# Performance work log

Hardware: AMD Instinct MI355X
Metric: run time of the kernel (lower is better)

Reference implementation:

```python
import jax, jax.numpy as jnp
import numpy as np

N, E, F, H, G = 50000, 800000, 128, 32, 64  # nodes, edges, feat, hidden, graphs


def _p(k, shape):
    return (jax.random.normal(k, shape, jnp.float32) / np.sqrt(shape[0])).astype(jnp.float32)


def setup_inputs() -> dict:
    key = jax.random.key(0)
    ks = jax.random.split(key, 24)
    x = jax.random.normal(ks[0], (N, F), jnp.float32)
    edge_index = jax.random.randint(ks[1], (2, E), 0, N, dtype=jnp.int32)
    batch = jnp.sort(jax.random.randint(ks[2], (N,), 0, G, dtype=jnp.int32))
    d = {"x": x, "edge_index": edge_index, "batch": batch}
    # GATv2 conv params: (Wl, Wr, att vector a, bias) per layer; dims 128->32->64->128
    dims = [(F, H), (H, 2 * H), (2 * H, 4 * H)]
    i = 3
    for li, (din, dout) in enumerate(dims, 1):
        d[f"Wl{li}"] = _p(ks[i], (din, dout)); i += 1
        d[f"Wr{li}"] = _p(ks[i], (din, dout)); i += 1
        d[f"a{li}"] = _p(ks[i], (dout,)); i += 1
        d[f"b{li}"] = jnp.zeros((dout,), jnp.float32)
    # MLP head 128->1024->512->128->32->4
    mdims = [(4 * H, 1024), (1024, 512), (512, 128), (128, 32), (32, 4)]
    for li, (din, dout) in enumerate(mdims, 1):
        d[f"mw{li}"] = _p(ks[i], (din, dout)); i += 1
        d[f"mb{li}"] = jnp.zeros((dout,), jnp.float32)
    return d


def _gatv2(x, Wl, Wr, a, b, src, dst, n):
    # GATv2: e = a . LeakyReLU(Wl x_src + Wr x_dst), softmax over incoming edges of dst
    xl = x @ Wl
    xr = x @ Wr
    e = jax.nn.leaky_relu(xl[src] + xr[dst], 0.2) @ a  # [E]
    m = jax.ops.segment_max(e, dst, num_segments=n)
    ex = jnp.exp(e - m[dst])
    denom = jax.ops.segment_sum(ex, dst, num_segments=n)
    alpha = ex / (denom[dst] + 1e-16)
    return jax.ops.segment_sum(alpha[:, None] * xl[src], dst, num_segments=n) + b


def reference(x, edge_index, batch,
              Wl1, Wr1, a1, b1, Wl2, Wr2, a2, b2, Wl3, Wr3, a3, b3,
              mw1, mb1, mw2, mb2, mw3, mb3, mw4, mb4, mw5, mb5):
    src, dst = edge_index[0], edge_index[1]
    n = x.shape[0]
    h = _gatv2(x, Wl1, Wr1, a1, b1, src, dst, n)
    h = jax.nn.leaky_relu(h, 0.01)
    h = _gatv2(h, Wl2, Wr2, a2, b2, src, dst, n)
    h = jax.nn.leaky_relu(h, 0.01)
    h = _gatv2(h, Wl3, Wr3, a3, b3, src, dst, n)
    # global max pool per graph
    g = jax.ops.segment_max(h, batch, num_segments=G)  # [G, 4H]
    g = jax.nn.relu(g @ mw1 + mb1)
    g = jax.nn.relu(g @ mw2 + mb2)
    g = jax.nn.relu(g @ mw3 + mb3)
    g = jax.nn.relu(g @ mw4 + mb4)
    return g @ mw5 + mb5  # [G, 4]
```

## Files before the change

kernel.cpp:

```cpp
#include <hip/hip_runtime.h>
#include <cfloat>

#define N_NODES 50000
#define N_EDGES 800000
#define N_GRAPHS 64
#define POOL_CHUNK 64
#define DEG_BUCKETS 64
#define SCAN_NB ((N_NODES + 255) / 256)

#define BUK_SHIFT 8
#define NBUK ((N_NODES + 255) / 256)
#define CHUNK 4096
#define CAP 6144

typedef _Float16 half8 __attribute__((ext_vector_type(8)));
typedef _Float16 half4 __attribute__((ext_vector_type(4)));


__global__ __launch_bounds__(256) void bucket_hist_kernel(const int* __restrict__ dst,
                                                          int* __restrict__ bhist, int n) {
    __shared__ int lh[NBUK];
    int t = threadIdx.x;
    if (t < NBUK) lh[t] = 0;
    __syncthreads();
    int i0 = blockIdx.x * 1024;
#pragma unroll
    for (int j = 0; j < 4; ++j) {
        int i = i0 + j * 256 + t;
        if (i < n) atomicAdd(&lh[dst[i] >> BUK_SHIFT], 1);
    }
    __syncthreads();
    if (t < NBUK && lh[t]) atomicAdd(&bhist[t], lh[t]);
}

__global__ __launch_bounds__(256) void bucket_scan_kernel(const int* __restrict__ bhist,
                                                          int* __restrict__ bbase,
                                                          int* __restrict__ bcur) {
    __shared__ int sm[256];
    int t = threadIdx.x;
    int v = (t < NBUK) ? bhist[t] : 0;
    sm[t] = v;
    __syncthreads();
    for (int off = 1; off < 256; off <<= 1) {
        int x = (t >= off) ? sm[t - off] : 0;
        __syncthreads();
        sm[t] += x;
        __syncthreads();
    }
    int excl = sm[t] - v;
    if (t < NBUK) { bbase[t] = excl; bcur[t] = excl; }
    if (t == 255) bbase[NBUK] = sm[255];
}


__global__ __launch_bounds__(256) void binscat_kernel(const int* __restrict__ src,
        const int* __restrict__ dst, int* __restrict__ bcur,
        int2* __restrict__ ebuf, int n) {
    __shared__ int2 staged[CHUNK];
    __shared__ int lh[NBUK], lbase[NBUK], lpos[NBUK], gpos[NBUK];
    __shared__ int ssc[256];
    int t = threadIdx.x;
    int e0 = blockIdx.x * CHUNK;
    int len = n - e0; if (len > CHUNK) len = CHUNK; if (len < 0) len = 0;
    if (t < NBUK) { lh[t] = 0; lpos[t] = 0; }
    __syncthreads();
    int s[16], d[16];
#pragma unroll
    for (int j = 0; j < 16; ++j) {
        int i = j * 256 + t;
        if (i < len) {
            s[j] = src[e0 + i];
            d[j] = dst[e0 + i];
            atomicAdd(&lh[d[j] >> BUK_SHIFT], 1);
        } else d[j] = -1;
    }
    __syncthreads();
    int v = (t < NBUK) ? lh[t] : 0;
    ssc[t] = v;
    __syncthreads();
    for (int off = 1; off < 256; off <<= 1) {
        int x = (t >= off) ? ssc[t - off] : 0;
        __syncthreads();
        ssc[t] += x;
        __syncthreads();
    }
    if (t < NBUK) {
        lbase[t] = ssc[t] - v;
        gpos[t] = v ? atomicAdd(&bcur[t], v) : 0;
    }
    __syncthreads();
#pragma unroll
    for (int j = 0; j < 16; ++j) {
        if (d[j] >= 0) {
            int b = d[j] >> BUK_SHIFT;
            int slot = lbase[b] + atomicAdd(&lpos[b], 1);
            staged[slot] = make_int2(s[j], d[j]);
        }
    }
    __syncthreads();
    for (int i = t; i < len; i += 256) {
        int2 p = staged[i];
        int b = p.y >> BUK_SHIFT;
        ebuf[gpos[b] + (i - lbase[b])] = p;
    }
}


__global__ __launch_bounds__(256) void csr_final_kernel(const int2* __restrict__ ebuf,
        const int* __restrict__ bbase, int* __restrict__ rowptr, int* __restrict__ csrc,
        int* __restrict__ deg, int* __restrict__ dhist, int n_nodes, int n_edges) {
    __shared__ int lcnt[256], lbs[256], lpos[256], ssc[256];
    __shared__ int lh64[DEG_BUCKETS];
    __shared__ int buf[CAP];
    int b = blockIdx.x, t = threadIdx.x;
    int nstart = b << BUK_SHIFT;
    int nodes = n_nodes - nstart; if (nodes > 256) nodes = 256;
    int r0 = bbase[b], r1 = bbase[b + 1];
    int len = r1 - r0;
    lcnt[t] = 0;
    lpos[t] = 0;
    if (t < DEG_BUCKETS) lh64[t] = 0;
    __syncthreads();
    for (int i = t; i < len; i += 256)
        atomicAdd(&lcnt[ebuf[r0 + i].y - nstart], 1);
    __syncthreads();
    int v = lcnt[t];
    ssc[t] = v;
    __syncthreads();
    for (int off = 1; off < 256; off <<= 1) {
        int x = (t >= off) ? ssc[t - off] : 0;
        __syncthreads();
        ssc[t] += x;
        __syncthreads();
    }
    lbs[t] = ssc[t] - v;
    if (t < nodes) {
        rowptr[nstart + t] = r0 + lbs[t];
        deg[nstart + t] = v;
        int dd = (v > DEG_BUCKETS - 1) ? DEG_BUCKETS - 1 : v;
        atomicAdd(&lh64[dd], 1);
    }
    if (b == NBUK - 1 && t == 0) rowptr[n_nodes] = n_edges;
    __syncthreads();
    if (t < DEG_BUCKETS && lh64[t]) atomicAdd(&dhist[t], lh64[t]);
    if (len <= CAP) {
        for (int i = t; i < len; i += 256) {
            int2 p = ebuf[r0 + i];
            int dn = p.y - nstart;
            int pos = lbs[dn] + atomicAdd(&lpos[dn], 1);
            buf[pos] = p.x;
        }
        __syncthreads();
        for (int i = t; i < len; i += 256) csrc[r0 + i] = buf[i];
    } else {
        for (int i = t; i < len; i += 256) {
            int2 p = ebuf[r0 + i];
            int dn = p.y - nstart;
            int pos = lbs[dn] + atomicAdd(&lpos[dn], 1);
            csrc[r0 + pos] = p.x;
        }
    }
}


__global__ void dscan_kernel(const int* __restrict__ dhist, int* __restrict__ dcur) {
    int t = threadIdx.x;
    int dv = dhist[t];
    int incl = dv;
    for (int off = 1; off < 64; off <<= 1) {
        int x = __shfl_up(incl, off, 64);
        if (t >= off) incl += x;
    }
    dcur[t] = incl - dv;
}

__global__ __launch_bounds__(256) void perm_kernel(const int* __restrict__ deg,
        int* __restrict__ dcur, int* __restrict__ perm, int n) {
    __shared__ int lh[DEG_BUCKETS], lbase[DEG_BUCKETS];
    int t = threadIdx.x;
    int i = blockIdx.x * 256 + t;
    if (t < DEG_BUCKETS) lh[t] = 0;
    __syncthreads();
    int d = 0, loc = 0;
    bool valid = (i < n);
    if (valid) {
        int v = deg[i];
        d = (v > DEG_BUCKETS - 1) ? DEG_BUCKETS - 1 : v;
        loc = atomicAdd(&lh[d], 1);
    }
    __syncthreads();
    if (t < DEG_BUCKETS) lbase[t] = lh[t] ? atomicAdd(&dcur[t], lh[t]) : 0;
    __syncthreads();
    if (valid) perm[lbase[d] + loc] = i;
}


template<int DIN, int DOUT, int TR, int RPT>
__global__ __launch_bounds__(256) void gemm2_kernel(const float* __restrict__ h,
        const float* __restrict__ Wl, const float* __restrict__ Wr,
        _Float16* __restrict__ xl, _Float16* __restrict__ xr, int n) {
    constexpr int CG = (2 * DOUT) / 4;
    constexpr int RG = 256 / CG;
    static_assert(RG * RPT == TR, "tile rows mismatch");
    static_assert(RPT % 4 == 0, "RPT multiple of 4");
    constexpr int TRP = TR + 4;
    __shared__ float sW[2 * DIN * DOUT];
    __shared__ float sX[DIN * TRP];
    int tid = threadIdx.x;
    for (int i = tid; i < DIN * DOUT; i += 256) {
        sW[i] = Wl[i];
        sW[DIN * DOUT + i] = Wr[i];
    }
    int r0 = blockIdx.x * TR;
    for (int i = tid; i < TR * DIN; i += 256) {
        int row = i / DIN, k = i % DIN;
        float v = (r0 + row < n) ? h[(r0 + row) * DIN + k] : 0.f;
        sX[k * TRP + row] = v;
    }
    __syncthreads();

    int cg = tid % CG, rg = tid / CG;
    int c = cg * 4;
    int sel = (c >= DOUT) ? 1 : 0;
    int cc = c - sel * DOUT;
    const float* wp = sW + sel * DIN * DOUT + cc;
    const float* xp = sX + rg * RPT;

    float acc[RPT][4] = {};
#pragma unroll 4
    for (int k = 0; k < DIN; ++k) {
        float4 wv = *(const float4*)(wp + k * DOUT);
        float wa[4] = {wv.x, wv.y, wv.z, wv.w};
        float xa[RPT];
#pragma unroll
        for (int rr = 0; rr < RPT; rr += 4) {
            float4 xv = *(const float4*)(xp + k * TRP + rr);
            xa[rr + 0] = xv.x; xa[rr + 1] = xv.y; xa[rr + 2] = xv.z; xa[rr + 3] = xv.w;
        }
#pragma unroll
        for (int r = 0; r < RPT; ++r)
#pragma unroll
            for (int q = 0; q < 4; ++q)
                acc[r][q] += xa[r] * wa[q];
    }

    _Float16* obase = sel ? xr : xl;
#pragma unroll
    for (int r = 0; r < RPT; ++r) {
        int row = r0 + rg * RPT + r;
        if (row < n) {
            half4 o = {(_Float16)acc[r][0], (_Float16)acc[r][1],
                       (_Float16)acc[r][2], (_Float16)acc[r][3]};
            *(half4*)(obase + (size_t)row * DOUT + cc) = o;
        }
    }
}

template<int DIN, int DOUT, int TR, int RPT>
__global__ __launch_bounds__(256) void gemm1w_kernel(const float* __restrict__ h,
        const float* __restrict__ Wl, const float* __restrict__ Wr,
        _Float16* __restrict__ xl, _Float16* __restrict__ xr, int n) {
    constexpr int CG = DOUT / 4;
    constexpr int RG = 256 / CG;
    static_assert(RG * RPT == TR, "tile rows mismatch");
    static_assert(RPT % 4 == 0, "RPT multiple of 4");
    constexpr int TRP = TR + 4;
    __shared__ float sW[DIN * DOUT];
    __shared__ float sX[DIN * TRP];
    int tid = threadIdx.x;
    int sel = blockIdx.x & 1;
    const float* W = sel ? Wr : Wl;
    for (int i = tid; i < DIN * DOUT; i += 256) sW[i] = W[i];
    int r0 = (blockIdx.x >> 1) * TR;
    for (int i = tid; i < TR * DIN; i += 256) {
        int row = i / DIN, k = i % DIN;
        float v = (r0 + row < n) ? h[(r0 + row) * DIN + k] : 0.f;
        sX[k * TRP + row] = v;
    }
    __syncthreads();

    int cg = tid % CG, rg = tid / CG;
    int cc = cg * 4;
    const float* wp = sW + cc;
    const float* xp = sX + rg * RPT;

    float acc[RPT][4] = {};
#pragma unroll 4
    for (int k = 0; k < DIN; ++k) {
        float4 wv = *(const float4*)(wp + k * DOUT);
        float wa[4] = {wv.x, wv.y, wv.z, wv.w};
        float xa[RPT];
#pragma unroll
        for (int rr = 0; rr < RPT; rr += 4) {
            float4 xv = *(const float4*)(xp + k * TRP + rr);
            xa[rr + 0] = xv.x; xa[rr + 1] = xv.y; xa[rr + 2] = xv.z; xa[rr + 3] = xv.w;
        }
#pragma unroll
        for (int r = 0; r < RPT; ++r)
#pragma unroll
            for (int q = 0; q < 4; ++q)
                acc[r][q] += xa[r] * wa[q];
    }

    _Float16* obase = sel ? xr : xl;
#pragma unroll
    for (int r = 0; r < RPT; ++r) {
        int row = r0 + rg * RPT + r;
        if (row < n) {
            half4 o = {(_Float16)acc[r][0], (_Float16)acc[r][1],
                       (_Float16)acc[r][2], (_Float16)acc[r][3]};
            *(half4*)(obase + (size_t)row * DOUT + cc) = o;
        }
    }
}


template<int DOUT, int U, bool LEAKY>
__global__ __launch_bounds__(256) void edge_kernel(
        const _Float16* __restrict__ xl, const _Float16* __restrict__ xr,
        const float* __restrict__ avec, const float* __restrict__ bias,
        const int* __restrict__ rowptr, const int* __restrict__ csrc,
        const int* __restrict__ perm,
        float* __restrict__ out, int n) {
    constexpr int LANES = DOUT / 8;
    constexpr int NPW = 64 / LANES;
    int wid = (blockIdx.x * blockDim.x + threadIdx.x) >> 6;
    int lane = threadIdx.x & 63;
    int group = lane / LANES;
    int gl = lane % LANES;
    int gnode = wid * NPW + group;
    if (gnode >= n) return;
    int node = perm[n - 1 - gnode];

    constexpr float L2E = 1.44269504f;
    float a6[8], a4[8];
    const float* ap = avec + 8 * gl;
#pragma unroll
    for (int i = 0; i < 8; ++i) {
        float av = ap[i];
        a6[i] = 0.6f * L2E * av;
        a4[i] = 0.4f * L2E * av;
    }

    int nbase = node * DOUT + 8 * gl;
    half8 xrh = *(const half8*)(xr + nbase);
    float xrv[8];
#pragma unroll
    for (int i = 0; i < 8; ++i) xrv[i] = (float)xrh[i];
    const _Float16* xlg = xl + 8 * gl;

    float acc[8] = {};
    float denom = 0.f;
    int e0 = rowptr[node], e1 = rowptr[node + 1];

    for (int p = e0; p < e1; p += U) {
        int sidx[U];
#pragma unroll
        for (int u = 0; u < U; ++u) {
            int q = p + u;
            sidx[u] = (q < e1) ? csrc[q] : -1;
        }
        half8 xlv[U];
#pragma unroll
        for (int u = 0; u < U; ++u) {
            int s = (sidx[u] >= 0) ? sidx[u] : 0;
            xlv[u] = *(const half8*)(xlg + (size_t)s * DOUT);
        }
        float part[U];
#pragma unroll
        for (int u = 0; u < U; ++u) {
            float pu = 0.f;
#pragma unroll
            for (int i = 0; i < 8; ++i) {
                float t = (float)xlv[u][i] + xrv[i];
                pu += a6[i] * t + a4[i] * fabsf(t);
            }
            part[u] = pu;
        }
#pragma unroll
        for (int mask = LANES / 2; mask >= 1; mask >>= 1)
#pragma unroll
            for (int u = 0; u < U; ++u)
                part[u] += __shfl_xor(part[u], mask, 64);
#pragma unroll
        for (int u = 0; u < U; ++u) {
            float w = __builtin_exp2f(part[u]);
            w = (sidx[u] >= 0) ? w : 0.f;
            denom += w;
#pragma unroll
            for (int i = 0; i < 8; ++i)
                acc[i] += w * (float)xlv[u][i];
        }
    }
    float inv = 1.f / (denom + 1e-16f);
    const float* bp = bias + 8 * gl;
    float o[8];
#pragma unroll
    for (int i = 0; i < 8; ++i) {
        float v = acc[i] * inv + bp[i];
        if (LEAKY) v = (v > 0.f) ? v : 0.01f * v;
        o[i] = v;
    }
    *(float4*)(out + nbase) = make_float4(o[0], o[1], o[2], o[3]);
    *(float4*)(out + nbase + 4) = make_float4(o[4], o[5], o[6], o[7]);
}


__device__ __forceinline__ unsigned int enc_f32(float f) {
    unsigned int b = __float_as_uint(f);
    return (b & 0x80000000u) ? ~b : (b | 0x80000000u);
}
__device__ __forceinline__ float dec_f32(unsigned int u) {
    unsigned int b = (u & 0x80000000u) ? (u ^ 0x80000000u) : ~u;
    return __uint_as_float(b);
}

__global__ __launch_bounds__(128) void pool_kernel(const float* __restrict__ h,
        const int* __restrict__ batch, unsigned int* __restrict__ gout, int n) {
    int c0 = blockIdx.x * POOL_CHUNK;
    if (c0 >= n) return;
    int end = c0 + POOL_CHUNK; if (end > n) end = n;
    int d = threadIdx.x;
    float run = -FLT_MAX;
    int gcur = batch[c0];
    for (int nn = c0; nn < end; ++nn) {
        int g = batch[nn];
        if (g != gcur) {
            atomicMax(&gout[gcur * 128 + d], enc_f32(run));
            run = -FLT_MAX;
            gcur = g;
        }
        run = fmaxf(run, h[nn * 128 + d]);
    }
    atomicMax(&gout[gcur * 128 + d], enc_f32(run));
}


__global__ __launch_bounds__(256) void mlp1_kernel(const unsigned int* __restrict__ gpool,
        const float* __restrict__ w1, const float* __restrict__ b1,
        float* __restrict__ act1) {
    __shared__ float A[128];
    int g = blockIdx.x >> 2, chunk = blockIdx.x & 3;
    int t = threadIdx.x;
    if (t < 128) A[t] = dec_f32(gpool[g * 128 + t]);
    __syncthreads();
    int c = chunk * 256 + t;
    float a0 = b1[c], a1 = 0.f;
#pragma unroll 4
    for (int k = 0; k < 128; k += 2) {
        a0 += A[k] * w1[k * 1024 + c];
        a1 += A[k + 1] * w1[(k + 1) * 1024 + c];
    }
    act1[g * 1024 + c] = fmaxf(a0 + a1, 0.f);
}

template<int DIN, int DOUT>
__global__ __launch_bounds__(256) void mlp_mid_kernel(const float* __restrict__ actin,
        const float* __restrict__ w, const float* __restrict__ b,
        float* __restrict__ actout) {
    constexpr int CHUNKS = DOUT / 64;
    constexpr int KQ = DIN / 4;
    __shared__ float A[DIN];
    __shared__ float partial[4][64];
    int g = blockIdx.x / CHUNKS, chunk = blockIdx.x % CHUNKS;
    int t = threadIdx.x;
    for (int i = t; i < DIN; i += 256) A[i] = actin[g * DIN + i];
    __syncthreads();
    int c = chunk * 64 + (t & 63);
    int q = t >> 6;
    const float* wp = w + c + (size_t)q * KQ * DOUT;
    const float* ap = A + q * KQ;
    float a0 = 0.f, a1 = 0.f;
#pragma unroll 4
    for (int k = 0; k < KQ; k += 2) {
        a0 += ap[k] * wp[k * DOUT];
        a1 += ap[k + 1] * wp[(k + 1) * DOUT];
    }
    partial[q][t & 63] = a0 + a1;
    __syncthreads();
    if (t < 64) {
        float s = partial[0][t] + partial[1][t] + partial[2][t] + partial[3][t] + b[c];
        actout[g * DOUT + chunk * 64 + t] = fmaxf(s, 0.f);
    }
}

__global__ __launch_bounds__(128) void mlp45_kernel(const float* __restrict__ act3,
        const float* __restrict__ w4, const float* __restrict__ b4,
        const float* __restrict__ w5, const float* __restrict__ b5,
        float* __restrict__ out) {
    __shared__ float C[128], D[32];
    int g = blockIdx.x, t = threadIdx.x;
    if (t < 128) C[t] = act3[g * 128 + t];
    __syncthreads();
    if (t < 32) {
        float acc = b4[t];
#pragma unroll 4
        for (int k = 0; k < 128; ++k) acc += C[k] * w4[k * 32 + t];
        D[t] = fmaxf(acc, 0.f);
    }
    __syncthreads();
    if (t < 4) {
        float acc = b5[t];
#pragma unroll
        for (int k = 0; k < 32; ++k) acc += D[k] * w5[k * 4 + t];
        out[g * 4 + t] = acc;
    }
}


extern "C" void kernel_launch(void* const* d_in, const int* in_sizes, int n_in,
                              void* d_out, int out_size, void* d_ws, size_t ws_size,
                              hipStream_t stream) {
    const float* x     = (const float*)d_in[0];
    const int*   ei    = (const int*)d_in[1];
    const int*   batch = (const int*)d_in[2];
    const int*   src   = ei;
    const int*   dst   = ei + N_EDGES;
    const float* Wl1 = (const float*)d_in[3];
    const float* Wr1 = (const float*)d_in[4];
    const float* a1  = (const float*)d_in[5];
    const float* b1  = (const float*)d_in[6];
    const float* Wl2 = (const float*)d_in[7];
    const float* Wr2 = (const float*)d_in[8];
    const float* a2  = (const float*)d_in[9];
    const float* b2  = (const float*)d_in[10];
    const float* Wl3 = (const float*)d_in[11];
    const float* Wr3 = (const float*)d_in[12];
    const float* a3  = (const float*)d_in[13];
    const float* b3  = (const float*)d_in[14];
    const float* mw1 = (const float*)d_in[15];
    const float* mb1 = (const float*)d_in[16];
    const float* mw2 = (const float*)d_in[17];
    const float* mb2 = (const float*)d_in[18];
    const float* mw3 = (const float*)d_in[19];
    const float* mb3 = (const float*)d_in[20];
    const float* mw4 = (const float*)d_in[21];
    const float* mb4 = (const float*)d_in[22];
    const float* mw5 = (const float*)d_in[23];
    const float* mb5 = (const float*)d_in[24];

    char* ws = (char*)d_ws;
    size_t off = 0;
    auto alloc = [&](size_t bytes) -> void* {
        void* p = ws + off;
        off = (off + bytes + 255) & ~(size_t)255;
        return p;
    };
    int*   bhist  = (int*)alloc(NBUK * 4);
    int*   dhist  = (int*)alloc(DEG_BUCKETS * 4);
    unsigned int* pool = (unsigned int*)alloc(N_GRAPHS * 128 * 4);
    size_t zero_bytes = off;
    int*   bbase  = (int*)alloc((NBUK + 1) * 4);
    int*   bcur   = (int*)alloc(NBUK * 4);
    int*   rowptr = (int*)alloc((N_NODES + 1) * 4);
    int*   csrc   = (int*)alloc(N_EDGES * 4);
    int2*  ebuf   = (int2*)alloc((size_t)N_EDGES * 8);
    _Float16* xl  = (_Float16*)alloc((size_t)N_NODES * 128 * 2);
    _Float16* xr  = (_Float16*)alloc((size_t)N_NODES * 128 * 2);
    float* hA     = (float*)alloc((size_t)N_NODES * 128 * 4);
    float* hB     = (float*)alloc((size_t)N_NODES * 128 * 4);
    int*   dcur   = (int*)alloc(DEG_BUCKETS * 4);
    int*   perm   = (int*)alloc(N_NODES * 4);
    int*   deg    = (int*)alloc(N_NODES * 4);
    float* act1   = (float*)alloc(N_GRAPHS * 1024 * 4);
    float* act2   = (float*)alloc(N_GRAPHS * 512 * 4);
    float* act3   = (float*)alloc(N_GRAPHS * 128 * 4);

    hipMemsetAsync(bhist, 0, zero_bytes, stream);
    bucket_hist_kernel<<<(N_EDGES + 1023) / 1024, 256, 0, stream>>>(dst, bhist, N_EDGES);
    bucket_scan_kernel<<<1, 256, 0, stream>>>(bhist, bbase, bcur);
    binscat_kernel<<<(N_EDGES + CHUNK - 1) / CHUNK, 256, 0, stream>>>(src, dst, bcur, ebuf, N_EDGES);
    csr_final_kernel<<<NBUK, 256, 0, stream>>>(ebuf, bbase, rowptr, csrc, deg, dhist, N_NODES, N_EDGES);
    dscan_kernel<<<1, 64, 0, stream>>>(dhist, dcur);
    perm_kernel<<<SCAN_NB, 256, 0, stream>>>(deg, dcur, perm, N_NODES);

    auto egrid = [](int npw) {
        int waves = (N_NODES + npw - 1) / npw;
        return (waves + 3) / 4;
    };

    gemm2_kernel<128, 32, 64, 4><<<(N_NODES + 63) / 64, 256, 0, stream>>>(x, Wl1, Wr1, xl, xr, N_NODES);
    edge_kernel<32, 16, true><<<egrid(16), 256, 0, stream>>>(xl, xr, a1, b1, rowptr, csrc, perm, hB, N_NODES);
    gemm2_kernel<32, 64, 32, 4><<<(N_NODES + 31) / 32, 256, 0, stream>>>(hB, Wl2, Wr2, xl, xr, N_NODES);
    edge_kernel<64, 16, true><<<egrid(8), 256, 0, stream>>>(xl, xr, a2, b2, rowptr, csrc, perm, hA, N_NODES);
    { int tiles = (N_NODES + 63) / 64;
      gemm1w_kernel<64, 128, 64, 8><<<2 * tiles, 256, 0, stream>>>(hA, Wl3, Wr3, xl, xr, N_NODES); }
    edge_kernel<128, 8, false><<<egrid(4), 256, 0, stream>>>(xl, xr, a3, b3, rowptr, csrc, perm, hB, N_NODES);

    pool_kernel<<<(N_NODES + POOL_CHUNK - 1) / POOL_CHUNK, 128, 0, stream>>>(hB, batch, pool, N_NODES);
    mlp1_kernel<<<N_GRAPHS * 4, 256, 0, stream>>>(pool, mw1, mb1, act1);
    mlp_mid_kernel<1024, 512><<<N_GRAPHS * 8, 256, 0, stream>>>(act1, mw2, mb2, act2);
    mlp_mid_kernel<512, 128><<<N_GRAPHS * 2, 256, 0, stream>>>(act2, mw3, mb3, act3);
    mlp45_kernel<<<N_GRAPHS, 128, 0, stream>>>(act3, mw4, mb4, mw5, mb5, (float*)d_out);
}
```

Measured before the change: 391.0 us.

## Replace FP32 SIMT node GEMMs with fp16 MFMA kernel using swizzled LDS

Replaces the two scalar FP32 register-tiled GEMM kernels that compute xl and xr with a single templated kernel built on the 16x16x32 fp16 MFMA instruction. Activations and weights are converted to fp16 in LDS with an XOR swizzle to avoid bank conflicts, and each wave computes a 16-row strip across all output columns. The aim is to cut the FMA-bound dense projection time in all three layers. Inputs are now rounded to fp16 before the multiply, which adds some precision loss, and the output stores become scalar fp16 writes instead of half4 vectors.

```diff
diff --git a/kernel.cpp b/kernel.cpp
--- a/kernel.cpp
+++ b/kernel.cpp
@@ -15,6 +15,8 @@
 
 typedef _Float16 half8 __attribute__((ext_vector_type(8)));
 typedef _Float16 half4 __attribute__((ext_vector_type(4)));
+typedef _Float16 f16x8 __attribute__((ext_vector_type(8)));
+typedef float f32x4 __attribute__((ext_vector_type(4)));
 
 
 __global__ __launch_bounds__(256) void bucket_hist_kernel(const int* __restrict__ dst,
@@ -195,121 +197,67 @@
 }
 
 
-template<int DIN, int DOUT, int TR, int RPT>
-__global__ __launch_bounds__(256) void gemm2_kernel(const float* __restrict__ h,
+template<int DIN, int DOUT>
+__global__ __launch_bounds__(256) void mfma_gemm_kernel(const float* __restrict__ h,
         const float* __restrict__ Wl, const float* __restrict__ Wr,
         _Float16* __restrict__ xl, _Float16* __restrict__ xr, int n) {
-    constexpr int CG = (2 * DOUT) / 4;
-    constexpr int RG = 256 / CG;
-    static_assert(RG * RPT == TR, "tile rows mismatch");
-    static_assert(RPT % 4 == 0, "RPT multiple of 4");
-    constexpr int TRP = TR + 4;
-    __shared__ float sW[2 * DIN * DOUT];
-    __shared__ float sX[DIN * TRP];
+    constexpr int NOUT = 2 * DOUT;
+    constexpr int BM = 64;
+    constexpr int NCH = DIN / 8;
+    constexpr int XORM = (NCH < 8 ? NCH : 8) - 1;
+    constexpr int NT = NOUT / 16;
+    static_assert(DIN % 32 == 0 && DOUT % 16 == 0, "shape");
+    __shared__ _Float16 sA[BM * DIN];
+    __shared__ _Float16 sW[NOUT * DIN];
     int tid = threadIdx.x;
+    int r0 = blockIdx.x * BM;
+
     for (int i = tid; i < DIN * DOUT; i += 256) {
-        sW[i] = Wl[i];
-        sW[DIN * DOUT + i] = Wr[i];
-    }
-    int r0 = blockIdx.x * TR;
-    for (int i = tid; i < TR * DIN; i += 256) {
-        int row = i / DIN, k = i % DIN;
-        float v = (r0 + row < n) ? h[(r0 + row) * DIN + k] : 0.f;
-        sX[k * TRP + row] = v;
-    }
-    __syncthreads();
-
-    int cg = tid % CG, rg = tid / CG;
-    int c = cg * 4;
-    int sel = (c >= DOUT) ? 1 : 0;
-    int cc = c - sel * DOUT;
-    const float* wp = sW + sel * DIN * DOUT + cc;
-    const float* xp = sX + rg * RPT;
-
-    float acc[RPT][4] = {};
-#pragma unroll 4
-    for (int k = 0; k < DIN; ++k) {
-        float4 wv = *(const float4*)(wp + k * DOUT);
-        float wa[4] = {wv.x, wv.y, wv.z, wv.w};
-        float xa[RPT];
-#pragma unroll
-        for (int rr = 0; rr < RPT; rr += 4) {
-            float4 xv = *(const float4*)(xp + k * TRP + rr);
-            xa[rr + 0] = xv.x; xa[rr + 1] = xv.y; xa[rr + 2] = xv.z; xa[rr + 3] = xv.w;
-        }
-#pragma unroll
-        for (int r = 0; r < RPT; ++r)
-#pragma unroll
-            for (int q = 0; q < 4; ++q)
-                acc[r][q] += xa[r] * wa[q];
-    }
-
-    _Float16* obase = sel ? xr : xl;
-#pragma unroll
-    for (int r = 0; r < RPT; ++r) {
-        int row = r0 + rg * RPT + r;
-        if (row < n) {
-            half4 o = {(_Float16)acc[r][0], (_Float16)acc[r][1],
-                       (_Float16)acc[r][2], (_Float16)acc[r][3]};
-            *(half4*)(obase + (size_t)row * DOUT + cc) = o;
-        }
-    }
-}
-
-template<int DIN, int DOUT, int TR, int RPT>
-__global__ __launch_bounds__(256) void gemm1w_kernel(const float* __restrict__ h,
-        const float* __restrict__ Wl, const float* __restrict__ Wr,
-        _Float16* __restrict__ xl, _Float16* __restrict__ xr, int n) {
-    constexpr int CG = DOUT / 4;
-    constexpr int RG = 256 / CG;
-    static_assert(RG * RPT == TR, "tile rows mismatch");
-    static_assert(RPT % 4 == 0, "RPT multiple of 4");
-    constexpr int TRP = TR + 4;
-    __shared__ float sW[DIN * DOUT];
-    __shared__ float sX[DIN * TRP];
-    int tid = threadIdx.x;
-    int sel = blockIdx.x & 1;
-    const float* W = sel ? Wr : Wl;
-    for (int i = tid; i < DIN * DOUT; i += 256) sW[i] = W[i];
-    int r0 = (blockIdx.x >> 1) * TR;
-    for (int i = tid; i < TR * DIN; i += 256) {
-        int row = i / DIN, k = i % DIN;
-        float v = (r0 + row < n) ? h[(r0 + row) * DIN + k] : 0.f;
-        sX[k * TRP + row] = v;
-    }
-    __syncthreads();
-
-    int cg = tid % CG, rg = tid / CG;
-    int cc = cg * 4;
-    const float* wp = sW + cc;
-    const float* xp = sX + rg * RPT;
-
-    float acc[RPT][4] = {};
-#pragma unroll 4
-    for (int k = 0; k < DIN; ++k) {
-        float4 wv = *(const float4*)(wp + k * DOUT);
-        float wa[4] = {wv.x, wv.y, wv.z, wv.w};
-        float xa[RPT];
-#pragma unroll
-        for (int rr = 0; rr < RPT; rr += 4) {
-            float4 xv = *(const float4*)(xp + k * TRP + rr);
-            xa[rr + 0] = xv.x; xa[rr + 1] = xv.y; xa[rr + 2] = xv.z; xa[rr + 3] = xv.w;
-        }
-#pragma unroll
-        for (int r = 0; r < RPT; ++r)
-#pragma unroll
-            for (int q = 0; q < 4; ++q)
-                acc[r][q] += xa[r] * wa[q];
-    }
-
-    _Float16* obase = sel ? xr : xl;
-#pragma unroll
-    for (int r = 0; r < RPT; ++r) {
-        int row = r0 + rg * RPT + r;
-        if (row < n) {
-            half4 o = {(_Float16)acc[r][0], (_Float16)acc[r][1],
-                       (_Float16)acc[r][2], (_Float16)acc[r][3]};
-            *(half4*)(obase + (size_t)row * DOUT + cc) = o;
+        int k = i / DOUT, c = i % DOUT;
+        sW[c * DIN + (k ^ ((c & XORM) << 3))] = (_Float16)Wl[i];
+        int nr = DOUT + c;
+        sW[nr * DIN + (k ^ ((nr & XORM) << 3))] = (_Float16)Wr[i];
+    }
+    constexpr int DQ = DIN / 4;
+    for (int i = tid; i < BM * DQ; i += 256) {
+        int row = i / DQ, kq = (i % DQ) * 4;
+        float4 v = (r0 + row < n) ? *(const float4*)(h + (size_t)(r0 + row) * DIN + kq)
+                                  : make_float4(0.f, 0.f, 0.f, 0.f);
+        half4 hv = {(_Float16)v.x, (_Float16)v.y, (_Float16)v.z, (_Float16)v.w};
+        *(half4*)(sA + row * DIN + (kq ^ ((row & XORM) << 3))) = hv;
+    }
+    __syncthreads();
+
+    int w = tid >> 6, lane = tid & 63;
+    int lrow = lane & 15, lg = lane >> 4;
+    int arow = w * 16 + lrow;
+
+    f32x4 acc[NT];
+#pragma unroll
+    for (int i = 0; i < NT; ++i) acc[i] = (f32x4){0.f, 0.f, 0.f, 0.f};
+
+#pragma unroll
+    for (int kk = 0; kk < DIN; kk += 32) {
+        int ka = kk + lg * 8;
+        f16x8 af = *(const f16x8*)(sA + arow * DIN + (ka ^ ((arow & XORM) << 3)));
+#pragma unroll
+        for (int nt = 0; nt < NT; ++nt) {
+            int bcol = nt * 16 + lrow;
+            f16x8 bf = *(const f16x8*)(sW + bcol * DIN + (ka ^ ((bcol & XORM) << 3)));
+            acc[nt] = __builtin_amdgcn_mfma_f32_16x16x32_f16(af, bf, acc[nt], 0, 0, 0);
+        }
+    }
+
+    int orow0 = r0 + w * 16 + lg * 4;
+#pragma unroll
+    for (int nt = 0; nt < NT; ++nt) {
+        int c = nt * 16 + lrow;
+        _Float16* obase = (c < DOUT) ? xl : xr;
+        int cc = (c < DOUT) ? c : c - DOUT;
+#pragma unroll
+        for (int r = 0; r < 4; ++r) {
+            int row = orow0 + r;
+            if (row < n) obase[(size_t)row * DOUT + cc] = (_Float16)acc[nt][r];
         }
     }
 }
@@ -578,13 +526,13 @@
         int waves = (N_NODES + npw - 1) / npw;
         return (waves + 3) / 4;
     };
-
-    gemm2_kernel<128, 32, 64, 4><<<(N_NODES + 63) / 64, 256, 0, stream>>>(x, Wl1, Wr1, xl, xr, N_NODES);
+    const int gblocks = (N_NODES + 63) / 64;
+
+    mfma_gemm_kernel<128, 32><<<gblocks, 256, 0, stream>>>(x, Wl1, Wr1, xl, xr, N_NODES);
     edge_kernel<32, 16, true><<<egrid(16), 256, 0, stream>>>(xl, xr, a1, b1, rowptr, csrc, perm, hB, N_NODES);
-    gemm2_kernel<32, 64, 32, 4><<<(N_NODES + 31) / 32, 256, 0, stream>>>(hB, Wl2, Wr2, xl, xr, N_NODES);
+    mfma_gemm_kernel<32, 64><<<gblocks, 256, 0, stream>>>(hB, Wl2, Wr2, xl, xr, N_NODES);
     edge_kernel<64, 16, true><<<egrid(8), 256, 0, stream>>>(xl, xr, a2, b2, rowptr, csrc, perm, hA, N_NODES);
-    { int tiles = (N_NODES + 63) / 64;
-      gemm1w_kernel<64, 128, 64, 8><<<2 * tiles, 256, 0, stream>>>(hA, Wl3, Wr3, xl, xr, N_NODES); }
+    mfma_gemm_kernel<64, 128><<<gblocks, 256, 0, stream>>>(hA, Wl3, Wr3, xl, xr, N_NODES);
     edge_kernel<128, 8, false><<<egrid(4), 256, 0, stream>>>(xl, xr, a3, b3, rowptr, csrc, perm, hB, N_NODES);
 
     pool_kernel<<<(N_NODES + POOL_CHUNK - 1) / POOL_CHUNK, 128, 0, stream>>>(hB, batch, pool, N_NODES);
```

Result: faster. 355.2 us (-9.2%).
